# Kernel tuning notes

Measured on AMD Instinct MI355X. Metric: run time of the kernel, lower is better.

Reference implementation:

```python
import jax, jax.numpy as jnp
import numpy as np

VOCAB, DIM = 50257, 128
B, R, C, T = 8, 100, 100, 20


def setup_inputs() -> dict:
    key = jax.random.key(0)
    k1, k2, k3 = jax.random.split(key, 3)
    x = jax.random.randint(k1, (B, R, C, T), 0, VOCAB, dtype=jnp.int32)
    emb = jax.random.normal(k2, (VOCAB, DIM), dtype=jnp.float32)
    W = jax.random.normal(k3, (DIM, 1), dtype=jnp.float32) / np.sqrt(DIM)
    b = jnp.zeros((1,), dtype=jnp.float32)
    return {"x": x, "emb": emb, "W": W, "b": b}


def reference(x, emb, W, b):
    # x: [B,R,C,T] int ids -> gather: [B,R,C,T,D]
    e = emb[x]
    # aggregate = mean over tokens (dropout is identity in eval)
    agg = e.mean(axis=-2)                      # [B,R,C,D]
    h = jax.nn.gelu(agg, approximate=False)    # exact erf GELU (torch default)
    logits = jnp.einsum('brcd,do->brc', h, W) + b[0]
    return logits                              # [B,R,C]
```

## Files before the change

kernel.cpp:

```cpp
#include <hip/hip_runtime.h>
#include <hip/hip_bf16.h>
#include <math.h>

constexpr int T_TOK  = 20;
constexpr int DIM    = 128;
constexpr int VOCAB  = 50257;
constexpr int NSLICE = 4;
constexpr int SDIM   = DIM / NSLICE;

__global__ __launch_bounds__(256) void convert_kernel(const float* __restrict__ emb,
                                                      ushort* __restrict__ embt)
{
    const int NWORK = VOCAB * (DIM / 8);
    int i = blockIdx.x * 256 + threadIdx.x;
    if (i >= NWORK) return;
    const int v  = i >> 4;
    const int j  = i & 15;
    const int s  = j >> 2;
    const int jj = j & 3;

    const float* src = emb + (size_t)v * DIM + j * 8;
    const float4 a = *reinterpret_cast<const float4*>(src);
    const float4 c = *reinterpret_cast<const float4*>(src + 4);

    auto pack2 = [](float lo, float hi) -> unsigned int {
        unsigned int l = __bfloat16_as_ushort(__float2bfloat16(lo));
        unsigned int h = __bfloat16_as_ushort(__float2bfloat16(hi));
        return l | (h << 16);
    };
    uint4 u;
    u.x = pack2(a.x, a.y);
    u.y = pack2(a.z, a.w);
    u.z = pack2(c.x, c.y);
    u.w = pack2(c.z, c.w);

    ushort* dst = embt + ((size_t)s * VOCAB + v) * SDIM + jj * 8;
    *reinterpret_cast<uint4*>(dst) = u;
}

__global__ __launch_bounds__(256) void gather_kernel(
    const int* __restrict__ x,
    const ushort* __restrict__ embt,
    const float* __restrict__ W,
    float* __restrict__ part,
    int n_out)
{
    const int s     = blockIdx.x & (NSLICE - 1);
    const int obase = (blockIdx.x >> 2) * 64;
    const int wv    = threadIdx.x >> 6;
    const int lane  = threadIdx.x & 63;
    const int g     = lane >> 2;
    const int j     = lane & 3;
    const int o     = obase + wv * 16 + g;
    if (o >= n_out) return;

    int ids_r[T_TOK];
    const int4* xp = reinterpret_cast<const int4*>(x + (size_t)o * T_TOK);
    #pragma unroll
    for (int q = 0; q < T_TOK / 4; ++q) {
        int4 t4 = xp[q];
        ids_r[4 * q + 0] = t4.x;
        ids_r[4 * q + 1] = t4.y;
        ids_r[4 * q + 2] = t4.z;
        ids_r[4 * q + 3] = t4.w;
    }

    const ushort* base = embt + (size_t)s * VOCAB * SDIM + j * 8;
    float acc[8] = {0.f, 0.f, 0.f, 0.f, 0.f, 0.f, 0.f, 0.f};

    #pragma unroll
    for (int t = 0; t < T_TOK; ++t) {
        const uint4 u = *reinterpret_cast<const uint4*>(base + (size_t)ids_r[t] * SDIM);
        acc[0] += __uint_as_float(u.x << 16);
        acc[1] += __uint_as_float(u.x & 0xffff0000u);
        acc[2] += __uint_as_float(u.y << 16);
        acc[3] += __uint_as_float(u.y & 0xffff0000u);
        acc[4] += __uint_as_float(u.z << 16);
        acc[5] += __uint_as_float(u.z & 0xffff0000u);
        acc[6] += __uint_as_float(u.w << 16);
        acc[7] += __uint_as_float(u.w & 0xffff0000u);
    }

    const float inv_t = 1.0f / (float)T_TOK;
    const float kInvSqrt2 = 0.70710678118654752440f;
    const float* wp = W + s * SDIM + j * 8;
    float p = 0.f;
    #pragma unroll
    for (int k = 0; k < 8; ++k) {
        const float a  = acc[k] * inv_t;
        const float gl = 0.5f * a * (1.0f + erff(a * kInvSqrt2));
        p += gl * wp[k];
    }

    p += __shfl_xor(p, 1, 64);
    p += __shfl_xor(p, 2, 64);
    if (j == 0)
        part[(size_t)s * n_out + o] = p;
}

__global__ __launch_bounds__(256) void reduce_kernel(const float* __restrict__ part,
                                                     const float* __restrict__ b,
                                                     float* __restrict__ out,
                                                     int n_out)
{
    int o = blockIdx.x * 256 + threadIdx.x;
    if (o >= n_out) return;
    float v = b[0];
    #pragma unroll
    for (int s = 0; s < NSLICE; ++s)
        v += part[(size_t)s * n_out + o];
    out[o] = v;
}

__global__ __launch_bounds__(256) void gelu_embed_fallback(
    const int* __restrict__ x, const float* __restrict__ emb,
    const float* __restrict__ W, const float* __restrict__ b,
    float* __restrict__ out, int n_out)
{
    const int wave = (int)((blockIdx.x * blockDim.x + threadIdx.x) >> 6);
    const int lane = (int)(threadIdx.x & 63);
    if (wave >= n_out) return;
    const int* ids = x + (size_t)wave * T_TOK;
    float2 acc = make_float2(0.f, 0.f);
    #pragma unroll
    for (int t = 0; t < T_TOK; ++t) {
        const int id = ids[t];
        const float2 v = *reinterpret_cast<const float2*>(
            emb + (size_t)id * DIM + (size_t)(lane * 2));
        acc.x += v.x; acc.y += v.y;
    }
    const float inv_t = 1.0f / (float)T_TOK;
    const float ax = acc.x * inv_t, ay = acc.y * inv_t;
    const float kInvSqrt2 = 0.70710678118654752440f;
    const float gx = 0.5f * ax * (1.0f + erff(ax * kInvSqrt2));
    const float gy = 0.5f * ay * (1.0f + erff(ay * kInvSqrt2));
    const float2 w = *reinterpret_cast<const float2*>(W + (size_t)(lane * 2));
    float p = gx * w.x + gy * w.y;
    #pragma unroll
    for (int off = 32; off >= 1; off >>= 1) p += __shfl_down(p, off, 64);
    if (lane == 0) out[wave] = p + b[0];
}

extern "C" void kernel_launch(void* const* d_in, const int* in_sizes, int n_in,
                              void* d_out, int out_size, void* d_ws, size_t ws_size,
                              hipStream_t stream) {
    const int*   x   = (const int*)d_in[0];
    const float* emb = (const float*)d_in[1];
    const float* W   = (const float*)d_in[2];
    const float* b   = (const float*)d_in[3];
    float* out = (float*)d_out;
    const int n_out = out_size;

    const size_t embt_bytes = (size_t)NSLICE * VOCAB * SDIM * sizeof(ushort);
    const size_t part_bytes = (size_t)NSLICE * n_out * sizeof(float);

    if (ws_size < embt_bytes + part_bytes) {
        const int blocks = (n_out + 3) / 4;
        gelu_embed_fallback<<<blocks, 256, 0, stream>>>(x, emb, W, b, out, n_out);
        return;
    }

    ushort* embt = (ushort*)d_ws;
    float*  part = (float*)((char*)d_ws + embt_bytes);

    {
        const int nwork  = VOCAB * (DIM / 8);
        const int blocks = (nwork + 255) / 256;
        convert_kernel<<<blocks, 256, 0, stream>>>(emb, embt);
    }
    {
        const int nchunk = (n_out + 63) / 64;
        gather_kernel<<<NSLICE * nchunk, 256, 0, stream>>>(x, embt, W, part, n_out);
    }
    {
        const int blocks = (n_out + 255) / 256;
        reduce_kernel<<<blocks, 256, 0, stream>>>(part, b, out, n_out);
    }
}
```

Before: 46.56 us.

## Pack token ids to 16-bit in convert pass and gather two outputs per thread

The convert kernel now also compresses the int32 token ids into 16-bit ids, since the vocabulary fits in 16 bits, and uses nontemporal loads and stores. The gather kernel reads these packed ids and handles two outputs per thread with two independent accumulator sets, which halves the id traffic and doubles the gather loads in flight. The extra conversion pass over x costs a read and a write. It also assumes n_ids is divisible by 8 and that each output's id row is 16-byte aligned, which holds for the test shape.

Result: slower. 56.14 us (+20.6%).

```diff
diff --git a/kernel.cpp b/kernel.cpp
--- a/kernel.cpp
+++ b/kernel.cpp
@@ -8,107 +8,127 @@
 constexpr int NSLICE = 4;
 constexpr int SDIM   = DIM / NSLICE;
 
-__global__ __launch_bounds__(256) void convert_kernel(const float* __restrict__ emb,
-                                                      ushort* __restrict__ embt)
-{
-    const int NWORK = VOCAB * (DIM / 8);
-    int i = blockIdx.x * 256 + threadIdx.x;
-    if (i >= NWORK) return;
-    const int v  = i >> 4;
-    const int j  = i & 15;
-    const int s  = j >> 2;
-    const int jj = j & 3;
-
-    const float* src = emb + (size_t)v * DIM + j * 8;
-    const float4 a = *reinterpret_cast<const float4*>(src);
-    const float4 c = *reinterpret_cast<const float4*>(src + 4);
-
-    auto pack2 = [](float lo, float hi) -> unsigned int {
-        unsigned int l = __bfloat16_as_ushort(__float2bfloat16(lo));
-        unsigned int h = __bfloat16_as_ushort(__float2bfloat16(hi));
-        return l | (h << 16);
-    };
-    uint4 u;
-    u.x = pack2(a.x, a.y);
-    u.y = pack2(a.z, a.w);
-    u.z = pack2(c.x, c.y);
-    u.w = pack2(c.z, c.w);
-
-    ushort* dst = embt + ((size_t)s * VOCAB + v) * SDIM + jj * 8;
-    *reinterpret_cast<uint4*>(dst) = u;
+typedef unsigned int  uint32x4 __attribute__((ext_vector_type(4)));
+typedef int           i32x4    __attribute__((ext_vector_type(4)));
+typedef float         f32x4    __attribute__((ext_vector_type(4)));
+typedef float         f32x2    __attribute__((ext_vector_type(2)));
+
+__global__ __launch_bounds__(256) void convert_kernel(
+    const float* __restrict__ emb, const int* __restrict__ x,
+    ushort* __restrict__ embt, ushort* __restrict__ ids16,
+    int nb_emb, int n_ids8)
+{
+    if ((int)blockIdx.x < nb_emb) {
+        const int i = blockIdx.x * 256 + threadIdx.x;
+        if (i >= VOCAB * (DIM / 8)) return;
+        const int v  = i >> 4;
+        const int jc = i & 15;
+        const int s  = jc >> 2;
+        const int jj = jc & 3;
+
+        const f32x4* src = reinterpret_cast<const f32x4*>(emb + (size_t)v * DIM + jc * 8);
+        const f32x4 a = __builtin_nontemporal_load(src);
+        const f32x4 c = __builtin_nontemporal_load(src + 1);
+
+        auto pack2 = [](float lo, float hi) -> unsigned int {
+            unsigned int l = __bfloat16_as_ushort(__float2bfloat16(lo));
+            unsigned int h = __bfloat16_as_ushort(__float2bfloat16(hi));
+            return l | (h << 16);
+        };
+        uint32x4 u = { pack2(a.x, a.y), pack2(a.z, a.w), pack2(c.x, c.y), pack2(c.z, c.w) };
+        ushort* dst = embt + ((size_t)s * VOCAB + v) * SDIM + jj * 8;
+        __builtin_nontemporal_store(u, reinterpret_cast<uint32x4*>(dst));
+    } else {
+        const int i = ((int)blockIdx.x - nb_emb) * 256 + threadIdx.x;
+        if (i >= n_ids8) return;
+        const i32x4* xp = reinterpret_cast<const i32x4*>(x) + (size_t)i * 2;
+        const i32x4 a = __builtin_nontemporal_load(xp);
+        const i32x4 c = __builtin_nontemporal_load(xp + 1);
+        uint32x4 u = { (unsigned)a.x | ((unsigned)a.y << 16),
+                       (unsigned)a.z | ((unsigned)a.w << 16),
+                       (unsigned)c.x | ((unsigned)c.y << 16),
+                       (unsigned)c.z | ((unsigned)c.w << 16) };
+        __builtin_nontemporal_store(u, reinterpret_cast<uint32x4*>(ids16 + (size_t)i * 8));
+    }
 }
 
 __global__ __launch_bounds__(256) void gather_kernel(
-    const int* __restrict__ x,
+    const ushort* __restrict__ ids16,
     const ushort* __restrict__ embt,
     const float* __restrict__ W,
     float* __restrict__ part,
     int n_out)
 {
     const int s     = blockIdx.x & (NSLICE - 1);
-    const int obase = (blockIdx.x >> 2) * 64;
-    const int wv    = threadIdx.x >> 6;
-    const int lane  = threadIdx.x & 63;
-    const int g     = lane >> 2;
-    const int j     = lane & 3;
-    const int o     = obase + wv * 16 + g;
-    if (o >= n_out) return;
-
-    int ids_r[T_TOK];
-    const int4* xp = reinterpret_cast<const int4*>(x + (size_t)o * T_TOK);
-    #pragma unroll
-    for (int q = 0; q < T_TOK / 4; ++q) {
-        int4 t4 = xp[q];
-        ids_r[4 * q + 0] = t4.x;
-        ids_r[4 * q + 1] = t4.y;
-        ids_r[4 * q + 2] = t4.z;
-        ids_r[4 * q + 3] = t4.w;
+    const int obase = ((int)blockIdx.x >> 2) * 128;
+    const int g     = threadIdx.x >> 2;
+    const int j     = threadIdx.x & 3;
+    const int o0    = obase + g * 2;
+    if (o0 >= n_out) return;
+
+    unsigned int idw[20];
+    {
+        const uint32x4* ip = reinterpret_cast<const uint32x4*>(ids16 + (size_t)o0 * T_TOK);
+        #pragma unroll
+        for (int q = 0; q < 5; ++q) {
+            uint32x4 u = __builtin_nontemporal_load(ip + q);
+            idw[4 * q + 0] = u.x; idw[4 * q + 1] = u.y;
+            idw[4 * q + 2] = u.z; idw[4 * q + 3] = u.w;
+        }
     }
 
     const ushort* base = embt + (size_t)s * VOCAB * SDIM + j * 8;
-    float acc[8] = {0.f, 0.f, 0.f, 0.f, 0.f, 0.f, 0.f, 0.f};
+    f32x2 accA[4] = {{0.f,0.f},{0.f,0.f},{0.f,0.f},{0.f,0.f}};
+    f32x2 accB[4] = {{0.f,0.f},{0.f,0.f},{0.f,0.f},{0.f,0.f}};
 
     #pragma unroll
     for (int t = 0; t < T_TOK; ++t) {
-        const uint4 u = *reinterpret_cast<const uint4*>(base + (size_t)ids_r[t] * SDIM);
-        acc[0] += __uint_as_float(u.x << 16);
-        acc[1] += __uint_as_float(u.x & 0xffff0000u);
-        acc[2] += __uint_as_float(u.y << 16);
-        acc[3] += __uint_as_float(u.y & 0xffff0000u);
-        acc[4] += __uint_as_float(u.z << 16);
-        acc[5] += __uint_as_float(u.z & 0xffff0000u);
-        acc[6] += __uint_as_float(u.w << 16);
-        acc[7] += __uint_as_float(u.w & 0xffff0000u);
+        const unsigned idA = (t & 1) ? (idw[t >> 1] >> 16)        : (idw[t >> 1] & 0xffffu);
+        const unsigned idB = (t & 1) ? (idw[10 + (t >> 1)] >> 16) : (idw[10 + (t >> 1)] & 0xffffu);
+        const uint32x4 uA = *reinterpret_cast<const uint32x4*>(base + (size_t)idA * SDIM);
+        const uint32x4 uB = *reinterpret_cast<const uint32x4*>(base + (size_t)idB * SDIM);
+        #pragma unroll
+        for (int q = 0; q < 4; ++q) {
+            f32x2 vA = { __uint_as_float(uA[q] << 16), __uint_as_float(uA[q] & 0xffff0000u) };
+            f32x2 vB = { __uint_as_float(uB[q] << 16), __uint_as_float(uB[q] & 0xffff0000u) };
+            accA[q] += vA;
+            accB[q] += vB;
+        }
     }
 
     const float inv_t = 1.0f / (float)T_TOK;
     const float kInvSqrt2 = 0.70710678118654752440f;
     const float* wp = W + s * SDIM + j * 8;
-    float p = 0.f;
+    const f32x4 w0 = *reinterpret_cast<const f32x4*>(wp);
+    const f32x4 w1 = *reinterpret_cast<const f32x4*>(wp + 4);
+    const float wv[8] = { w0.x, w0.y, w0.z, w0.w, w1.x, w1.y, w1.z, w1.w };
+
+    float pA = 0.f, pB = 0.f;
     #pragma unroll
     for (int k = 0; k < 8; ++k) {
-        const float a  = acc[k] * inv_t;
-        const float gl = 0.5f * a * (1.0f + erff(a * kInvSqrt2));
-        p += gl * wp[k];
-    }
-
-    p += __shfl_xor(p, 1, 64);
-    p += __shfl_xor(p, 2, 64);
-    if (j == 0)
-        part[(size_t)s * n_out + o] = p;
+        const float aA = accA[k >> 1][k & 1] * inv_t;
+        const float aB = accB[k >> 1][k & 1] * inv_t;
+        pA += 0.5f * aA * (1.0f + erff(aA * kInvSqrt2)) * wv[k];
+        pB += 0.5f * aB * (1.0f + erff(aB * kInvSqrt2)) * wv[k];
+    }
+
+    pA += __shfl_xor(pA, 1, 64);  pB += __shfl_xor(pB, 1, 64);
+    pA += __shfl_xor(pA, 2, 64);  pB += __shfl_xor(pB, 2, 64);
+
+    if (j == 0) __builtin_nontemporal_store(pA, part + (size_t)s * n_out + o0);
+    if (j == 1) __builtin_nontemporal_store(pB, part + (size_t)s * n_out + o0 + 1);
 }
 
 __global__ __launch_bounds__(256) void reduce_kernel(const float* __restrict__ part,
                                                      const float* __restrict__ b,
-                                                     float* __restrict__ out,
-                                                     int n_out)
-{
-    int o = blockIdx.x * 256 + threadIdx.x;
+                                                     float* __restrict__ out, int n_out)
+{
+    const int o = blockIdx.x * 256 + threadIdx.x;
     if (o >= n_out) return;
     float v = b[0];
     #pragma unroll
     for (int s = 0; s < NSLICE; ++s)
-        v += part[(size_t)s * n_out + o];
+        v += __builtin_nontemporal_load(part + (size_t)s * n_out + o);
     out[o] = v;
 }
 
@@ -150,27 +170,32 @@
     const float* b   = (const float*)d_in[3];
     float* out = (float*)d_out;
     const int n_out = out_size;
+    const int n_ids = n_out * T_TOK;
 
     const size_t embt_bytes = (size_t)NSLICE * VOCAB * SDIM * sizeof(ushort);
+    const size_t ids_bytes  = (size_t)n_ids * sizeof(ushort);
     const size_t part_bytes = (size_t)NSLICE * n_out * sizeof(float);
 
-    if (ws_size < embt_bytes + part_bytes) {
+    if (ws_size < embt_bytes + ids_bytes + part_bytes) {
         const int blocks = (n_out + 3) / 4;
         gelu_embed_fallback<<<blocks, 256, 0, stream>>>(x, emb, W, b, out, n_out);
         return;
     }
 
-    ushort* embt = (ushort*)d_ws;
-    float*  part = (float*)((char*)d_ws + embt_bytes);
-
-    {
-        const int nwork  = VOCAB * (DIM / 8);
-        const int blocks = (nwork + 255) / 256;
-        convert_kernel<<<blocks, 256, 0, stream>>>(emb, embt);
-    }
-    {
-        const int nchunk = (n_out + 63) / 64;
-        gather_kernel<<<NSLICE * nchunk, 256, 0, stream>>>(x, embt, W, part, n_out);
+    ushort* embt  = (ushort*)d_ws;
+    ushort* ids16 = (ushort*)((char*)d_ws + embt_bytes);
+    float*  part  = (float*)((char*)d_ws + embt_bytes + ids_bytes);
+
+    {
+        const int nb_emb = (VOCAB * (DIM / 8) + 255) / 256;
+        const int n_ids8 = n_ids / 8;
+        const int nb_ids = (n_ids8 + 255) / 256;
+        convert_kernel<<<nb_emb + nb_ids, 256, 0, stream>>>(emb, x, embt, ids16,
+                                                            nb_emb, n_ids8);
+    }
+    {
+        const int nchunk = (n_out + 127) / 128;
+        gather_kernel<<<NSLICE * nchunk, 256, 0, stream>>>(ids16, embt, W, part, n_out);
     }
     {
         const int blocks = (n_out + 255) / 256;
```

## Replace reduce pass with atomics and split tokens across lane pairs

Applied to the files above, without the earlier changes.

The separate reduce kernel is removed. The bias initialisation of the output is folded into the convert kernel's grid, and the gather kernel now accumulates slice partials directly into the output with relaxed atomics. Each output's 20 tokens are split between two 4-lane groups that are combined by a shuffle, which doubles the number of threads per output and the number of independent gathers in flight. Packed float2 accumulation is used so the compiler can emit packed adds. This saves a launch and the partial-buffer traffic, at the cost of atomic contention (four adds per output) and an order-dependent float sum.

New measurement: 49.66 us. 6.7% more time.

```diff
diff --git a/kernel.cpp b/kernel.cpp
--- a/kernel.cpp
+++ b/kernel.cpp
@@ -8,78 +8,81 @@
 constexpr int NSLICE = 4;
 constexpr int SDIM   = DIM / NSLICE;
 
-__global__ __launch_bounds__(256) void convert_kernel(const float* __restrict__ emb,
-                                                      ushort* __restrict__ embt)
+typedef unsigned int  uint32x4 __attribute__((ext_vector_type(4)));
+typedef float         f32x2    __attribute__((ext_vector_type(2)));
+
+__global__ __launch_bounds__(256) void convert_kernel(
+    const float* __restrict__ emb, const float* __restrict__ b,
+    ushort* __restrict__ embt, float* __restrict__ out,
+    int nb_emb, int n_out)
 {
-    const int NWORK = VOCAB * (DIM / 8);
-    int i = blockIdx.x * 256 + threadIdx.x;
-    if (i >= NWORK) return;
-    const int v  = i >> 4;
-    const int j  = i & 15;
-    const int s  = j >> 2;
-    const int jj = j & 3;
+    if ((int)blockIdx.x < nb_emb) {
+        const int i = blockIdx.x * 256 + threadIdx.x;
+        if (i >= VOCAB * (DIM / 8)) return;
+        const int v  = i >> 4;
+        const int jc = i & 15;
+        const int s  = jc >> 2;
+        const int jj = jc & 3;
 
-    const float* src = emb + (size_t)v * DIM + j * 8;
-    const float4 a = *reinterpret_cast<const float4*>(src);
-    const float4 c = *reinterpret_cast<const float4*>(src + 4);
+        const float* src = emb + (size_t)v * DIM + jc * 8;
+        const float4 a = *reinterpret_cast<const float4*>(src);
+        const float4 c = *reinterpret_cast<const float4*>(src + 4);
 
-    auto pack2 = [](float lo, float hi) -> unsigned int {
-        unsigned int l = __bfloat16_as_ushort(__float2bfloat16(lo));
-        unsigned int h = __bfloat16_as_ushort(__float2bfloat16(hi));
-        return l | (h << 16);
-    };
-    uint4 u;
-    u.x = pack2(a.x, a.y);
-    u.y = pack2(a.z, a.w);
-    u.z = pack2(c.x, c.y);
-    u.w = pack2(c.z, c.w);
-
-    ushort* dst = embt + ((size_t)s * VOCAB + v) * SDIM + jj * 8;
-    *reinterpret_cast<uint4*>(dst) = u;
+        auto pack2 = [](float lo, float hi) -> unsigned int {
+            unsigned int l = __bfloat16_as_ushort(__float2bfloat16(lo));
+            unsigned int h = __bfloat16_as_ushort(__float2bfloat16(hi));
+            return l | (h << 16);
+        };
+        uint32x4 u = { pack2(a.x, a.y), pack2(a.z, a.w), pack2(c.x, c.y), pack2(c.z, c.w) };
+        *reinterpret_cast<uint32x4*>(embt + ((size_t)s * VOCAB + v) * SDIM + jj * 8) = u;
+    } else {
+        const int i = ((int)blockIdx.x - nb_emb) * 256 + threadIdx.x;
+        if (i < n_out) out[i] = b[0];
+    }
 }
 
 __global__ __launch_bounds__(256) void gather_kernel(
     const int* __restrict__ x,
     const ushort* __restrict__ embt,
     const float* __restrict__ W,
-    float* __restrict__ part,
+    float* __restrict__ out,
     int n_out)
 {
-    const int s     = blockIdx.x & (NSLICE - 1);
-    const int obase = (blockIdx.x >> 2) * 64;
-    const int wv    = threadIdx.x >> 6;
-    const int lane  = threadIdx.x & 63;
-    const int g     = lane >> 2;
-    const int j     = lane & 3;
-    const int o     = obase + wv * 16 + g;
+    const int s = blockIdx.x & (NSLICE - 1);
+    const int o = ((int)blockIdx.x >> 2) * 32 + ((int)threadIdx.x >> 3);
+    const int h = ((int)threadIdx.x >> 2) & 1;
+    const int j = threadIdx.x & 3;
     if (o >= n_out) return;
 
-    int ids_r[T_TOK];
-    const int4* xp = reinterpret_cast<const int4*>(x + (size_t)o * T_TOK);
-    #pragma unroll
-    for (int q = 0; q < T_TOK / 4; ++q) {
-        int4 t4 = xp[q];
-        ids_r[4 * q + 0] = t4.x;
-        ids_r[4 * q + 1] = t4.y;
-        ids_r[4 * q + 2] = t4.z;
-        ids_r[4 * q + 3] = t4.w;
+    const int* xo = x + (size_t)o * T_TOK;
+    int ids[10];
+    {
+        const int4 a = *reinterpret_cast<const int4*>(xo + (h ? 12 : 0));
+        const int4 c = *reinterpret_cast<const int4*>(xo + (h ? 16 : 4));
+        const int2 e = *reinterpret_cast<const int2*>(xo + (h ? 10 : 8));
+        ids[0] = a.x; ids[1] = a.y; ids[2] = a.z; ids[3] = a.w;
+        ids[4] = c.x; ids[5] = c.y; ids[6] = c.z; ids[7] = c.w;
+        ids[8] = e.x; ids[9] = e.y;
     }
 
     const ushort* base = embt + (size_t)s * VOCAB * SDIM + j * 8;
-    float acc[8] = {0.f, 0.f, 0.f, 0.f, 0.f, 0.f, 0.f, 0.f};
+    f32x2 acc[4] = {{0.f,0.f},{0.f,0.f},{0.f,0.f},{0.f,0.f}};
 
     #pragma unroll
-    for (int t = 0; t < T_TOK; ++t) {
-        const uint4 u = *reinterpret_cast<const uint4*>(base + (size_t)ids_r[t] * SDIM);
-        acc[0] += __uint_as_float(u.x << 16);
-        acc[1] += __uint_as_float(u.x & 0xffff0000u);
-        acc[2] += __uint_as_float(u.y << 16);
-        acc[3] += __uint_as_float(u.y & 0xffff0000u);
-        acc[4] += __uint_as_float(u.z << 16);
-        acc[5] += __uint_as_float(u.z & 0xffff0000u);
-        acc[6] += __uint_as_float(u.w << 16);
-        acc[7] += __uint_as_float(u.w & 0xffff0000u);
+    for (int t = 0; t < 10; ++t) {
+        const uint32x4 u = *reinterpret_cast<const uint32x4*>(base + (size_t)ids[t] * SDIM);
+        #pragma unroll
+        for (int q = 0; q < 4; ++q) {
+            f32x2 v = { __uint_as_float(u[q] << 16), __uint_as_float(u[q] & 0xffff0000u) };
+            acc[q] += v;
+        }
     }
+
+    float accf[8] = { acc[0].x, acc[0].y, acc[1].x, acc[1].y,
+                      acc[2].x, acc[2].y, acc[3].x, acc[3].y };
+    #pragma unroll
+    for (int k = 0; k < 8; ++k)
+        accf[k] += __shfl_xor(accf[k], 4, 64);
 
     const float inv_t = 1.0f / (float)T_TOK;
     const float kInvSqrt2 = 0.70710678118654752440f;
@@ -87,29 +90,15 @@
     float p = 0.f;
     #pragma unroll
     for (int k = 0; k < 8; ++k) {
-        const float a  = acc[k] * inv_t;
-        const float gl = 0.5f * a * (1.0f + erff(a * kInvSqrt2));
-        p += gl * wp[k];
+        const float a  = accf[k] * inv_t;
+        p += 0.5f * a * (1.0f + erff(a * kInvSqrt2)) * wp[k];
     }
 
     p += __shfl_xor(p, 1, 64);
     p += __shfl_xor(p, 2, 64);
-    if (j == 0)
-        part[(size_t)s * n_out + o] = p;
-}
 
-__global__ __launch_bounds__(256) void reduce_kernel(const float* __restrict__ part,
-                                                     const float* __restrict__ b,
-                                                     float* __restrict__ out,
-                                                     int n_out)
-{
-    int o = blockIdx.x * 256 + threadIdx.x;
-    if (o >= n_out) return;
-    float v = b[0];
-    #pragma unroll
-    for (int s = 0; s < NSLICE; ++s)
-        v += part[(size_t)s * n_out + o];
-    out[o] = v;
+    if ((threadIdx.x & 7) == 0)
+        __hip_atomic_fetch_add(out + o, p, __ATOMIC_RELAXED, __HIP_MEMORY_SCOPE_AGENT);
 }
 
 __global__ __launch_bounds__(256) void gelu_embed_fallback(
@@ -152,28 +141,23 @@
     const int n_out = out_size;
 
     const size_t embt_bytes = (size_t)NSLICE * VOCAB * SDIM * sizeof(ushort);
-    const size_t part_bytes = (size_t)NSLICE * n_out * sizeof(float);
 
-    if (ws_size < embt_bytes + part_bytes) {
+    if (ws_size < embt_bytes) {
         const int blocks = (n_out + 3) / 4;
         gelu_embed_fallback<<<blocks, 256, 0, stream>>>(x, emb, W, b, out, n_out);
         return;
     }
 
     ushort* embt = (ushort*)d_ws;
-    float*  part = (float*)((char*)d_ws + embt_bytes);
 
     {
-        const int nwork  = VOCAB * (DIM / 8);
-        const int blocks = (nwork + 255) / 256;
-        convert_kernel<<<blocks, 256, 0, stream>>>(emb, embt);
+        const int nb_emb = (VOCAB * (DIM / 8) + 255) / 256;
+        const int nb_out = (n_out + 255) / 256;
+        convert_kernel<<<nb_emb + nb_out, 256, 0, stream>>>(emb, b, embt, out,
+                                                            nb_emb, n_out);
     }
     {
-        const int nchunk = (n_out + 63) / 64;
-        gather_kernel<<<NSLICE * nchunk, 256, 0, stream>>>(x, embt, W, part, n_out);
-    }
-    {
-        const int blocks = (n_out + 255) / 256;
-        reduce_kernel<<<blocks, 256, 0, stream>>>(part, b, out, n_out);
+        const int nchunk = (n_out + 31) / 32;
+        gather_kernel<<<NSLICE * nchunk, 256, 0, stream>>>(x, embt, W, out, n_out);
     }
 }
```
